# Kernel tuning notes

Measured on AMD Instinct MI355X. Metric: run time of the kernel, lower is better.

The kernel has to match this reference:

```python
import jax, jax.numpy as jnp
import numpy as np

TAU = 1.0
EPS = 1e-8  # F.cosine_similarity default eps


def _normalize(v):
    n = jnp.sqrt(jnp.sum(v * v, axis=-1, keepdims=True))
    return v / jnp.maximum(n, EPS)


def _compute_cl(X, Y):
    # cosine-sim matrix via normalize + matmul (same math as broadcasted
    # F.cosine_similarity, without the (bs,bs,hidden) intermediate)
    S = _normalize(X) @ _normalize(Y).T            # (bs, bs), S[i,j] = cos(X_i, Y_j)
    E = jnp.exp(S / TAU)                            # (bs, bs)
    pos = jnp.diagonal(E)                           # (bs,) exp(diag/tau)
    neg = jnp.sum(E, axis=0) - pos                  # (bs,) column sums minus diagonal
    return (-jnp.log(pos / neg))[:, None]           # (bs, 1) — torch's view(bs, -1)


def setup_inputs() -> dict:
    key = jax.random.key(0)
    kx, ky = jax.random.split(key)
    X = jax.random.normal(kx, (8192, 2048), dtype=jnp.float32)
    Y = jax.random.normal(ky, (8192, 2048), dtype=jnp.float32)
    return {"X": X, "Y": Y}


def reference(X, Y):
    return _compute_cl(X, Y) + _compute_cl(Y, X)
```

## Files before the change

kernel.cpp:

```cpp
#include <hip/hip_runtime.h>
#include <hip/hip_bf16.h>
#include <math.h>

typedef float f32x4 __attribute__((ext_vector_type(4)));
typedef int   i32x4 __attribute__((ext_vector_type(4)));
typedef int   i32x8 __attribute__((ext_vector_type(8)));

#define BSZ 8192
#define DIM 2048
#define NTILE 64
#define ROWB (DIM / 2)
#define BKB 128
#define KSTEPS 8

#define SCALE_I32 0x79797979

__device__ __forceinline__ unsigned f2fp4(float v) {
  float a = fabsf(v);
  unsigned s = (__float_as_uint(v) >> 31) << 3;
  unsigned m = (a < 0.25f) ? 0u
             : (a < 0.75f) ? 1u
             : (a < 1.25f) ? 2u
             : (a < 1.75f) ? 3u
             : (a < 2.5f)  ? 4u
             : (a < 3.5f)  ? 5u
             : (a < 5.0f)  ? 6u : 7u;
  return s | m;
}

__global__ void __launch_bounds__(256) k_prep(const float* __restrict__ X,
                                              const float* __restrict__ Y,
                                              unsigned char* __restrict__ Xq,
                                              unsigned char* __restrict__ Yq,
                                              float* __restrict__ dg) {
  const int row = blockIdx.x;
  const int tid = threadIdx.x;
  const float4* xp = (const float4*)(X + (size_t)row * DIM);
  const float4* yp = (const float4*)(Y + (size_t)row * DIM);
  float4 x0 = xp[tid * 2], x1 = xp[tid * 2 + 1];
  float4 y0 = yp[tid * 2], y1 = yp[tid * 2 + 1];
  float sxx = x0.x*x0.x + x0.y*x0.y + x0.z*x0.z + x0.w*x0.w
            + x1.x*x1.x + x1.y*x1.y + x1.z*x1.z + x1.w*x1.w;
  float syy = y0.x*y0.x + y0.y*y0.y + y0.z*y0.z + y0.w*y0.w
            + y1.x*y1.x + y1.y*y1.y + y1.z*y1.z + y1.w*y1.w;
  float sxy = x0.x*y0.x + x0.y*y0.y + x0.z*y0.z + x0.w*y0.w
            + x1.x*y1.x + x1.y*y1.y + x1.z*y1.z + x1.w*y1.w;
#pragma unroll
  for (int m = 32; m >= 1; m >>= 1) {
    sxx += __shfl_xor(sxx, m);
    syy += __shfl_xor(syy, m);
    sxy += __shfl_xor(sxy, m);
  }
  __shared__ float sh[3][4];
  if ((tid & 63) == 0) {
    sh[0][tid >> 6] = sxx; sh[1][tid >> 6] = syy; sh[2][tid >> 6] = sxy;
  }
  __syncthreads();
  float xx = sh[0][0] + sh[0][1] + sh[0][2] + sh[0][3];
  float yy = sh[1][0] + sh[1][1] + sh[1][2] + sh[1][3];
  float xy = sh[2][0] + sh[2][1] + sh[2][2] + sh[2][3];
  float nx = fmaxf(sqrtf(xx), 1e-8f);
  float ny = fmaxf(sqrtf(yy), 1e-8f);
  float ix = 64.0f / nx, iy = 64.0f / ny;
  float vx[8] = {x0.x, x0.y, x0.z, x0.w, x1.x, x1.y, x1.z, x1.w};
  float vy[8] = {y0.x, y0.y, y0.z, y0.w, y1.x, y1.y, y1.z, y1.w};
  unsigned ux = 0, uy = 0;
#pragma unroll
  for (int i = 0; i < 8; ++i) {
    ux |= f2fp4(vx[i] * ix) << (4 * i);
    uy |= f2fp4(vy[i] * iy) << (4 * i);
  }
  *(unsigned*)(Xq + (size_t)row * ROWB + tid * 4) = ux;
  *(unsigned*)(Yq + (size_t)row * ROWB + tid * 4) = uy;
  if (tid == 0) dg[row] = xy / (nx * ny);
}

__global__ void __launch_bounds__(256) k_gemm(const unsigned char* __restrict__ Xq,
                                              const unsigned char* __restrict__ Yq,
                                              float* __restrict__ rowpart,
                                              float* __restrict__ colpart) {
  const int bm = blockIdx.x & (NTILE - 1);
  const int bn = blockIdx.x >> 6;
  const int tileRow = bm * 128;
  const int tileCol = bn * 128;

  __shared__ __align__(16) unsigned char As[128][BKB];
  __shared__ __align__(16) unsigned char Bs[128][BKB];
  __shared__ float rsum2[2][128];
  __shared__ float csum2[2][128];

  const int tid = threadIdx.x;
  const int lane = tid & 63;
  const int w = tid >> 6;
  const int wr = w >> 1;
  const int wc = w & 1;
  const int lo = lane & 15;
  const int hi = lane >> 4;

  f32x4 acc[4][4];
#pragma unroll
  for (int m = 0; m < 4; ++m)
#pragma unroll
    for (int n = 0; n < 4; ++n) acc[m][n] = (f32x4){0.f, 0.f, 0.f, 0.f};

  const size_t lrow = (size_t)(lane >> 3);
  const int    lcol = (((lane & 7) ^ (lane >> 3)) * 16);
  const unsigned char* gxa = Xq + ((size_t)(tileRow + w * 32) + lrow) * ROWB + lcol;
  const unsigned char* gyb = Yq + ((size_t)(tileCol + w * 32) + lrow) * ROWB + lcol;

  for (int t = 0; t < KSTEPS; ++t) {
    const int kbase = t * BKB;
#pragma unroll
    for (int i = 0; i < 4; ++i) {
      __builtin_amdgcn_global_load_lds(
          (const __attribute__((address_space(1))) void*)(gxa + (size_t)i * 8 * ROWB + kbase),
          (__attribute__((address_space(3))) void*)&As[w * 32 + i * 8][0],
          16, 0, 0);
      __builtin_amdgcn_global_load_lds(
          (const __attribute__((address_space(1))) void*)(gyb + (size_t)i * 8 * ROWB + kbase),
          (__attribute__((address_space(3))) void*)&Bs[w * 32 + i * 8][0],
          16, 0, 0);
    }
    __syncthreads();

#pragma unroll
    for (int kk = 0; kk < 2; ++kk) {
      i32x4 a[4], b[4];
#pragma unroll
      for (int m = 0; m < 4; ++m)
        a[m] = *(const i32x4*)&As[wr * 64 + m * 16 + lo][((kk * 4 + hi) ^ (lo & 7)) * 16];
#pragma unroll
      for (int n = 0; n < 4; ++n)
        b[n] = *(const i32x4*)&Bs[wc * 64 + n * 16 + lo][((kk * 4 + hi) ^ (lo & 7)) * 16];
#pragma unroll
      for (int m = 0; m < 4; ++m) {
        i32x8 av = {a[m][0], a[m][1], a[m][2], a[m][3], 0, 0, 0, 0};
#pragma unroll
        for (int n = 0; n < 4; ++n) {
          i32x8 bv = {b[n][0], b[n][1], b[n][2], b[n][3], 0, 0, 0, 0};
          acc[m][n] = __builtin_amdgcn_mfma_scale_f32_16x16x128_f8f6f4(
              av, bv, acc[m][n],
              4, 4,
              0, SCALE_I32,
              0, SCALE_I32);
        }
      }
    }
    __syncthreads();
  }

  float rp[4][4];
  float cp[4];
#pragma unroll
  for (int m = 0; m < 4; ++m)
#pragma unroll
    for (int q = 0; q < 4; ++q) rp[m][q] = 0.f;
#pragma unroll
  for (int n = 0; n < 4; ++n) cp[n] = 0.f;

#pragma unroll
  for (int m = 0; m < 4; ++m)
#pragma unroll
    for (int n = 0; n < 4; ++n)
#pragma unroll
      for (int q = 0; q < 4; ++q) {
        float e = __expf(acc[m][n][q]);
        rp[m][q] += e;
        cp[n] += e;
      }

#pragma unroll
  for (int m = 0; m < 4; ++m)
#pragma unroll
    for (int q = 0; q < 4; ++q) {
      float v = rp[m][q];
      v += __shfl_xor(v, 1);
      v += __shfl_xor(v, 2);
      v += __shfl_xor(v, 4);
      v += __shfl_xor(v, 8);
      rp[m][q] = v;
    }
#pragma unroll
  for (int n = 0; n < 4; ++n) {
    float v = cp[n];
    v += __shfl_xor(v, 16);
    v += __shfl_xor(v, 32);
    cp[n] = v;
  }

  if (lo == 0) {
#pragma unroll
    for (int m = 0; m < 4; ++m)
#pragma unroll
      for (int q = 0; q < 4; ++q)
        rsum2[wc][wr * 64 + m * 16 + hi * 4 + q] = rp[m][q];
  }
  if (hi == 0) {
#pragma unroll
    for (int n = 0; n < 4; ++n)
      csum2[wr][wc * 64 + n * 16 + lo] = cp[n];
  }
  __syncthreads();

  if (tid < 128) {
    rowpart[(size_t)bn * BSZ + tileRow + tid] = rsum2[0][tid] + rsum2[1][tid];
    colpart[(size_t)bm * BSZ + tileCol + tid] = csum2[0][tid] + csum2[1][tid];
  }
}

__global__ void __launch_bounds__(256) k_final(const float* __restrict__ rowpart,
                                               const float* __restrict__ colpart,
                                               const float* __restrict__ dg,
                                               float* __restrict__ out) {
  const int k = blockIdx.x * 256 + threadIdx.x;
  float rs = 0.f, cs = 0.f;
#pragma unroll 8
  for (int s = 0; s < NTILE; ++s) {
    rs += rowpart[(size_t)s * BSZ + k];
    cs += colpart[(size_t)s * BSZ + k];
  }
  float d = dg[k];
  float p = __expf(d);
  out[k] = logf(cs - p) + logf(rs - p) - 2.0f * d;
}

extern "C" void kernel_launch(void* const* d_in, const int* in_sizes, int n_in,
                              void* d_out, int out_size, void* d_ws, size_t ws_size,
                              hipStream_t stream) {
  const float* X = (const float*)d_in[0];
  const float* Y = (const float*)d_in[1];
  float* out = (float*)d_out;

  char* ws = (char*)d_ws;
  unsigned char* Xq = (unsigned char*)ws;
  unsigned char* Yq = (unsigned char*)(ws + (size_t)BSZ * ROWB);
  float* diag = (float*)(ws + (size_t)BSZ * ROWB * 2);
  float* rowpart = (float*)(ws + (size_t)BSZ * ROWB * 2 + BSZ * 4);
  float* colpart = (float*)(ws + (size_t)BSZ * ROWB * 2 + BSZ * 4 + (size_t)NTILE * BSZ * 4);

  k_prep<<<BSZ, 256, 0, stream>>>(X, Y, Xq, Yq, diag);
  k_gemm<<<NTILE * NTILE, 256, 0, stream>>>(Xq, Yq, rowpart, colpart);
  k_final<<<BSZ / 256, 256, 0, stream>>>(rowpart, colpart, diag, out);
}
```

Measured before the change: 134.3 us.

## Pre-swizzle FP4 operands into MFMA fragment layout and load directly to registers

The prep kernel now writes quantized FP4 data in a blocked layout that matches the MFMA 16x16x128 operand fragments, so each lane can fetch its fragment with one coalesced 16-byte global load. The GEMM kernel drops the LDS staging buffers and barriers and double-buffers fragments in registers across 16 K-groups. This removes LDS traffic and synchronisation, but cross-wave reuse through shared memory is lost, so every wave reads its operands from global memory or cache directly.

```diff
diff --git a/kernel.cpp b/kernel.cpp
--- a/kernel.cpp
+++ b/kernel.cpp
@@ -9,11 +9,10 @@
 #define BSZ 8192
 #define DIM 2048
 #define NTILE 64
-#define ROWB (DIM / 2)
-#define BKB 128
-#define KSTEPS 8
+#define NKG 16
 
 #define SCALE_I32 0x79797979
+
 
 __device__ __forceinline__ unsigned f2fp4(float v) {
   float a = fabsf(v);
@@ -70,8 +69,13 @@
     ux |= f2fp4(vx[i] * ix) << (4 * i);
     uy |= f2fp4(vy[i] * iy) << (4 * i);
   }
-  *(unsigned*)(Xq + (size_t)row * ROWB + tid * 4) = ux;
-  *(unsigned*)(Yq + (size_t)row * ROWB + tid * 4) = uy;
+  const unsigned kkg = tid >> 4;
+  const unsigned hi4 = (tid >> 2) & 3;
+  const unsigned byt = (tid & 3) * 4;
+  const unsigned R = row >> 4, lo16 = row & 15;
+  const size_t addr = (((size_t)(kkg << 9) + R) << 10) + (hi4 * 16 + lo16) * 16 + byt;
+  *(unsigned*)(Xq + addr) = ux;
+  *(unsigned*)(Yq + addr) = uy;
   if (tid == 0) dg[row] = xy / (nx * ny);
 }
 
@@ -84,8 +88,6 @@
   const int tileRow = bm * 128;
   const int tileCol = bn * 128;
 
-  __shared__ __align__(16) unsigned char As[128][BKB];
-  __shared__ __align__(16) unsigned char Bs[128][BKB];
   __shared__ float rsum2[2][128];
   __shared__ float csum2[2][128];
 
@@ -103,51 +105,45 @@
 #pragma unroll
     for (int n = 0; n < 4; ++n) acc[m][n] = (f32x4){0.f, 0.f, 0.f, 0.f};
 
-  const size_t lrow = (size_t)(lane >> 3);
-  const int    lcol = (((lane & 7) ^ (lane >> 3)) * 16);
-  const unsigned char* gxa = Xq + ((size_t)(tileRow + w * 32) + lrow) * ROWB + lcol;
-  const unsigned char* gyb = Yq + ((size_t)(tileCol + w * 32) + lrow) * ROWB + lcol;
-
-  for (int t = 0; t < KSTEPS; ++t) {
-    const int kbase = t * BKB;
-#pragma unroll
-    for (int i = 0; i < 4; ++i) {
-      __builtin_amdgcn_global_load_lds(
-          (const __attribute__((address_space(1))) void*)(gxa + (size_t)i * 8 * ROWB + kbase),
-          (__attribute__((address_space(3))) void*)&As[w * 32 + i * 8][0],
-          16, 0, 0);
-      __builtin_amdgcn_global_load_lds(
-          (const __attribute__((address_space(1))) void*)(gyb + (size_t)i * 8 * ROWB + kbase),
-          (__attribute__((address_space(3))) void*)&Bs[w * 32 + i * 8][0],
-          16, 0, 0);
-    }
-    __syncthreads();
-
-#pragma unroll
-    for (int kk = 0; kk < 2; ++kk) {
-      i32x4 a[4], b[4];
-#pragma unroll
-      for (int m = 0; m < 4; ++m)
-        a[m] = *(const i32x4*)&As[wr * 64 + m * 16 + lo][((kk * 4 + hi) ^ (lo & 7)) * 16];
-#pragma unroll
-      for (int n = 0; n < 4; ++n)
-        b[n] = *(const i32x4*)&Bs[wc * 64 + n * 16 + lo][((kk * 4 + hi) ^ (lo & 7)) * 16];
-#pragma unroll
-      for (int m = 0; m < 4; ++m) {
-        i32x8 av = {a[m][0], a[m][1], a[m][2], a[m][3], 0, 0, 0, 0};
-#pragma unroll
-        for (int n = 0; n < 4; ++n) {
-          i32x8 bv = {b[n][0], b[n][1], b[n][2], b[n][3], 0, 0, 0, 0};
-          acc[m][n] = __builtin_amdgcn_mfma_scale_f32_16x16x128_f8f6f4(
-              av, bv, acc[m][n],
-              4, 4,
-              0, SCALE_I32,
-              0, SCALE_I32);
-        }
-      }
-    }
-    __syncthreads();
-  }
+  const unsigned char* Ab = Xq + (((size_t)(bm * 8 + wr * 4)) << 10) + lane * 16;
+  const unsigned char* Bb = Yq + (((size_t)(bn * 8 + wc * 4)) << 10) + lane * 16;
+
+#define LOADF(da, db, g) do {                                                  \
+    const unsigned char* pa_ = Ab + ((size_t)(g) << 19);                       \
+    const unsigned char* pb_ = Bb + ((size_t)(g) << 19);                       \
+    da[0] = *(const i32x4*)(pa_);                                              \
+    da[1] = *(const i32x4*)(pa_ + 1024);                                       \
+    da[2] = *(const i32x4*)(pa_ + 2048);                                       \
+    da[3] = *(const i32x4*)(pa_ + 3072);                                       \
+    db[0] = *(const i32x4*)(pb_);                                              \
+    db[1] = *(const i32x4*)(pb_ + 1024);                                       \
+    db[2] = *(const i32x4*)(pb_ + 2048);                                       \
+    db[3] = *(const i32x4*)(pb_ + 3072);                                       \
+  } while (0)
+
+#define MM(aa, bb) do {                                                        \
+    _Pragma("unroll")                                                          \
+    for (int m_ = 0; m_ < 4; ++m_) {                                           \
+      i32x8 av_ = {aa[m_][0], aa[m_][1], aa[m_][2], aa[m_][3], 0, 0, 0, 0};    \
+      _Pragma("unroll")                                                        \
+      for (int n_ = 0; n_ < 4; ++n_) {                                         \
+        i32x8 bv_ = {bb[n_][0], bb[n_][1], bb[n_][2], bb[n_][3], 0, 0, 0, 0};  \
+        acc[m_][n_] = __builtin_amdgcn_mfma_scale_f32_16x16x128_f8f6f4(        \
+            av_, bv_, acc[m_][n_], 4, 4, 0, SCALE_I32, 0, SCALE_I32);          \
+      }                                                                        \
+    }                                                                          \
+  } while (0)
+
+  i32x4 a0[4], b0[4], a1[4], b1[4];
+  LOADF(a0, b0, 0);
+  for (int g = 0; g < NKG; g += 2) {
+    LOADF(a1, b1, g + 1);
+    MM(a0, b0);
+    if (g + 2 < NKG) LOADF(a0, b0, g + 2);
+    MM(a1, b1);
+  }
+#undef LOADF
+#undef MM
 
   float rp[4][4];
   float cp[4];
@@ -233,10 +229,10 @@
 
   char* ws = (char*)d_ws;
   unsigned char* Xq = (unsigned char*)ws;
-  unsigned char* Yq = (unsigned char*)(ws + (size_t)BSZ * ROWB);
-  float* diag = (float*)(ws + (size_t)BSZ * ROWB * 2);
-  float* rowpart = (float*)(ws + (size_t)BSZ * ROWB * 2 + BSZ * 4);
-  float* colpart = (float*)(ws + (size_t)BSZ * ROWB * 2 + BSZ * 4 + (size_t)NTILE * BSZ * 4);
+  unsigned char* Yq = (unsigned char*)(ws + (size_t)BSZ * DIM / 2);
+  float* diag = (float*)(ws + (size_t)BSZ * DIM);
+  float* rowpart = (float*)(ws + (size_t)BSZ * DIM + BSZ * 4);
+  float* colpart = (float*)(ws + (size_t)BSZ * DIM + BSZ * 4 + (size_t)NTILE * BSZ * 4);
 
   k_prep<<<BSZ, 256, 0, stream>>>(X, Y, Xq, Yq, diag);
   k_gemm<<<NTILE * NTILE, 256, 0, stream>>>(Xq, Yq, rowpart, colpart);
```

Result: faster. 127.7 us (-4.9%).
